# Performance work log

Measured on AMD Instinct MI355X. Metric: run time of the kernel, lower is better.

The kernel has to match this reference:

```python
import jax, jax.numpy as jnp
import numpy as np

B, T, DIM = 2, 2048, 1024
H, HKV, D = 16, 4, 64
ROPE_DIMS = 32
ROPE_BASE = 10000.0


def fake_quant(w, n_bits):
    # per-output-row absmax symmetric fake quantization with STE
    half = 2 ** (n_bits - 1)
    w_max = jnp.maximum(jnp.max(jnp.abs(w), axis=1, keepdims=True), 1e-5)
    w_int = jnp.clip(jnp.round(w / w_max * half), -half, half - 1)
    w_q = w_int / half * w_max
    return w + jax.lax.stop_gradient(w_q - w)


def rms_norm(x):
    eps = jnp.finfo(x.dtype).eps
    return x * jax.lax.rsqrt(jnp.mean(x * x, axis=-1, keepdims=True) + eps)


def rope_tables(seq_len, dtype):
    inv_freq = 1.0 / (ROPE_BASE ** (jnp.arange(0, ROPE_DIMS, 2, dtype=jnp.float32) / ROPE_DIMS))
    t = jnp.arange(seq_len, dtype=jnp.float32)
    freqs = t[:, None] * inv_freq[None, :]  # [T, rope_dims/2]
    return jnp.cos(freqs).astype(dtype)[None, None], jnp.sin(freqs).astype(dtype)[None, None]


def apply_rotary(x, cos, sin):
    # partial rotary: rotate first ROPE_DIMS dims, pass the rest through
    x_rope, x_pass = x[..., :ROPE_DIMS], x[..., ROPE_DIMS:]
    half = ROPE_DIMS // 2
    x1, x2 = x_rope[..., :half], x_rope[..., half:]
    rot = jnp.concatenate([x1 * cos + x2 * sin, -x1 * sin + x2 * cos], axis=-1)
    return jnp.concatenate([rot, x_pass], axis=-1)


def setup_inputs() -> dict:
    key = jax.random.key(0)
    ks = jax.random.split(key, 5)
    kv_dim = HKV * D
    return {
        "x": jax.random.normal(ks[0], (B, T, DIM), dtype=jnp.float32),
        "w_q": jax.random.normal(ks[1], (DIM, DIM), dtype=jnp.float32) * 0.02,
        "w_k": jax.random.normal(ks[2], (kv_dim, DIM), dtype=jnp.float32) * 0.02,
        "w_v": jax.random.normal(ks[3], (kv_dim, DIM), dtype=jnp.float32) * 0.02,
        "w_proj": jax.random.normal(ks[4], (DIM, DIM), dtype=jnp.float32) * 0.02,
        "q_gain": jnp.full((H,), 1.5, dtype=jnp.float32),
    }


def reference(x, w_q, w_k, w_v, w_proj, q_gain):
    bsz, seqlen, dim = x.shape
    group = H // HKV

    # quantized (STE) projections
    q = x @ fake_quant(w_q, 6).T        # [B, T, DIM]
    k = x @ fake_quant(w_k, 6).T        # [B, T, HKV*D]
    v = x @ fake_quant(w_v, 5).T        # [B, T, HKV*D]

    q = q.reshape(bsz, seqlen, H, D).transpose(0, 2, 1, 3)    # [B, H, T, D]
    k = k.reshape(bsz, seqlen, HKV, D).transpose(0, 2, 1, 3)  # [B, HKV, T, D]
    v = v.reshape(bsz, seqlen, HKV, D).transpose(0, 2, 1, 3)  # [B, HKV, T, D]

    q = rms_norm(q)
    k = rms_norm(k)

    cos, sin = rope_tables(seqlen, q.dtype)
    q = apply_rotary(q, cos, sin)
    k = apply_rotary(k, cos, sin)

    q = q * q_gain.astype(q.dtype)[None, :, None, None]

    # grouped-query causal attention; scores kept in grouped [B,HKV,g,T,T] layout
    qg = q.reshape(bsz, HKV, group, seqlen, D)
    scores = jnp.einsum('bhgqd,bhkd->bhgqk', qg, k) / jnp.sqrt(jnp.asarray(D, q.dtype))
    causal = jnp.tril(jnp.ones((seqlen, seqlen), dtype=bool))
    scores = jnp.where(causal[None, None, None], scores, jnp.asarray(-jnp.inf, scores.dtype))
    att = jax.nn.softmax(scores, axis=-1)
    y = jnp.einsum('bhgqk,bhkd->bhgqd', att, v)               # [B, HKV, g, T, D]

    # xsa: orthogonalize y against normalized v (per kv head group)
    y_g = y.transpose(0, 3, 1, 2, 4)                           # [B, T, HKV, g, D]
    v_t = v.transpose(0, 2, 1, 3)                              # [B, T, HKV, D]
    vn = v_t / jnp.maximum(jnp.linalg.norm(v_t, axis=-1, keepdims=True), 1e-12)
    vn = vn[..., None, :]                                      # [B, T, HKV, 1, D]
    proj = jnp.sum(y_g * vn, axis=-1, keepdims=True) * vn
    y_out = (y_g - proj).reshape(bsz, seqlen, dim)

    return y_out @ fake_quant(w_proj, 5).T
```

## Files before the change

kernel.cpp:

```cpp
#include <hip/hip_runtime.h>
#include <math.h>

typedef unsigned short u16;
typedef __attribute__((ext_vector_type(8))) short short8;
typedef __attribute__((ext_vector_type(4))) float float4v;
typedef __attribute__((ext_vector_type(4))) u16 ushort4v;

namespace {
constexpr int kT    = 2048;
constexpr int kDim  = 1024;
constexpr int kH    = 16;
constexpr int kHKV  = 4;
constexpr int kD    = 64;
constexpr int kTok  = 4096;
constexpr int kQKVN = 1536;
}

__device__ __forceinline__ u16 f2bf(float f) {
  unsigned int u = __builtin_bit_cast(unsigned int, f);
  u = (u + 0x7FFFu + ((u >> 16) & 1u)) >> 16;
  return (u16)u;
}

__global__ __launch_bounds__(256) void prep_kernel(
    const float* __restrict__ x,
    const float* __restrict__ w_q, const float* __restrict__ w_k,
    const float* __restrict__ w_v, const float* __restrict__ w_proj,
    u16* __restrict__ xb, u16* __restrict__ wqkv, u16* __restrict__ wpq,
    float2* __restrict__ ropetab)
{
  __shared__ float red[4];
  const int bid = blockIdx.x, tid = threadIdx.x;

  if (bid < 128) {
    const int idx = bid * 256 + tid;
    const int t = idx >> 4, i = idx & 15;
    const float fr = (float)t * powf(10000.0f, -(float)i * (1.0f / 16.0f));
    ropetab[idx] = make_float2(cosf(fr), sinf(fr));
    return;
  }
  if (bid < 2176) {
    const size_t i = ((size_t)(bid - 128) * 256 + tid) * 8;
    const float4 a = *(const float4*)(x + i);
    const float4 b = *(const float4*)(x + i + 4);
    short8 r;
    r[0] = (short)f2bf(a.x); r[1] = (short)f2bf(a.y);
    r[2] = (short)f2bf(a.z); r[3] = (short)f2bf(a.w);
    r[4] = (short)f2bf(b.x); r[5] = (short)f2bf(b.y);
    r[6] = (short)f2bf(b.z); r[7] = (short)f2bf(b.w);
    *(short8*)(xb + i) = r;
    return;
  }
  const int rid = bid - 2176;
  const float* src; u16* dst; float halfv;
  if (rid < 1024)      { src = w_q    + (size_t)rid * 1024;          dst = wqkv + (size_t)rid * 1024;          halfv = 32.0f; }
  else if (rid < 1280) { src = w_k    + (size_t)(rid - 1024) * 1024; dst = wqkv + (size_t)rid * 1024;          halfv = 32.0f; }
  else if (rid < 1536) { src = w_v    + (size_t)(rid - 1280) * 1024; dst = wqkv + (size_t)rid * 1024;          halfv = 16.0f; }
  else                 { src = w_proj + (size_t)(rid - 1536) * 1024; dst = wpq  + (size_t)(rid - 1536) * 1024; halfv = 16.0f; }

  const float4 v4 = *(const float4*)(src + tid * 4);
  float mx = fmaxf(fmaxf(fabsf(v4.x), fabsf(v4.y)), fmaxf(fabsf(v4.z), fabsf(v4.w)));
  #pragma unroll
  for (int m = 1; m < 64; m <<= 1) mx = fmaxf(mx, __shfl_xor(mx, m));
  if ((tid & 63) == 0) red[tid >> 6] = mx;
  __syncthreads();
  mx = fmaxf(fmaxf(red[0], red[1]), fmaxf(red[2], red[3]));
  const float wmax = fmaxf(mx, 1e-5f);
  const float inv_half = 1.0f / halfv;
  const float vals[4] = {v4.x, v4.y, v4.z, v4.w};
  ushort4v o;
  #pragma unroll
  for (int j = 0; j < 4; ++j) {
    float r = rintf(vals[j] / wmax * halfv);
    r = fminf(fmaxf(r, -halfv), halfv - 1.0f);
    o[j] = f2bf(r * inv_half * wmax);
  }
  *(ushort4v*)(dst + tid * 4) = o;
}

#define GEMM_CORE(A_, W_, K_, NCOL0_)                                          \
  __shared__ u16 As[128][32];                                                  \
  __shared__ u16 Bs[64][32];                                                   \
  const int tid = threadIdx.x;                                                 \
  const int lane = tid & 63, wv = tid >> 6;                                    \
  const int n = lane & 15, quad = lane >> 4;                                   \
  const int wm = wv * 32;                                                      \
  const int m0 = blockIdx.y * 128;                                             \
  const int sr = tid >> 2, sc = (tid & 3) * 8;                                 \
  const int scs = sc ^ ((sr & 3) * 8);                                         \
  float4v acc[2][4];                                                           \
  _Pragma("unroll")                                                            \
  for (int mi = 0; mi < 2; ++mi)                                               \
    _Pragma("unroll")                                                          \
    for (int ni = 0; ni < 4; ++ni) {                                           \
      acc[mi][ni][0]=0.f; acc[mi][ni][1]=0.f;                                  \
      acc[mi][ni][2]=0.f; acc[mi][ni][3]=0.f; }                                \
  short8 a0r, a1r, b0r;                                                        \
  a0r = *(const short8*)(A_ + (size_t)(m0 + sr) * K_ + sc);                    \
  a1r = *(const short8*)(A_ + (size_t)(m0 + sr + 64) * K_ + sc);               \
  b0r = *(const short8*)(W_ + (size_t)(NCOL0_ + sr) * K_ + sc);                \
  for (int k0 = 0; k0 < K_; k0 += 32) {                                        \
    __syncthreads();                                                           \
    *(short8*)&As[sr][scs] = a0r;  *(short8*)&As[sr + 64][scs] = a1r;          \
    *(short8*)&Bs[sr][scs] = b0r;                                              \
    __syncthreads();                                                           \
    if (k0 + 32 < K_) {                                                        \
      a0r = *(const short8*)(A_ + (size_t)(m0 + sr) * K_ + k0 + 32 + sc);      \
      a1r = *(const short8*)(A_ + (size_t)(m0 + sr + 64) * K_ + k0 + 32 + sc); \
      b0r = *(const short8*)(W_ + (size_t)(NCOL0_ + sr) * K_ + k0 + 32 + sc);  \
    }                                                                          \
    short8 af[2], bf[4];                                                       \
    _Pragma("unroll")                                                          \
    for (int mi = 0; mi < 2; ++mi)                                             \
      af[mi] = *(const short8*)&As[wm + mi * 16 + n][(quad * 8) ^ ((n & 3) * 8)]; \
    _Pragma("unroll")                                                          \
    for (int ni = 0; ni < 4; ++ni)                                             \
      bf[ni] = *(const short8*)&Bs[ni * 16 + n][(quad * 8) ^ ((n & 3) * 8)];   \
    _Pragma("unroll")                                                          \
    for (int mi = 0; mi < 2; ++mi)                                             \
      _Pragma("unroll")                                                        \
      for (int ni = 0; ni < 4; ++ni)                                           \
        acc[mi][ni] = __builtin_amdgcn_mfma_f32_16x16x32_bf16(af[mi], bf[ni], acc[mi][ni], 0, 0, 0); \
  }

__global__ __launch_bounds__(256) void gemm_qkv(
    const u16* __restrict__ A, const u16* __restrict__ W,
    const float2* __restrict__ ropetab, const float* __restrict__ q_gain,
    u16* __restrict__ qh, u16* __restrict__ kh,
    u16* __restrict__ vT, float* __restrict__ vcmp)
{
  GEMM_CORE(A, W, kDim, (int)(blockIdx.x * 64))

  const int p = blockIdx.x;
  const int rbase = m0 + wm;
  const int bI = rbase >> 11;

  if (p < 20) {
    const float gain = (p < 16) ? q_gain[p] * 0.125f : 1.0f;
    u16* dst = (p < 16) ? qh + ((size_t)(bI * kH + p) * kT) * kD
                        : kh + ((size_t)(bI * kHKV + (p - 16)) * kT) * kD;
    #pragma unroll
    for (int mi = 0; mi < 2; ++mi)
      #pragma unroll
      for (int i = 0; i < 4; ++i) {
        const int row = rbase + mi * 16 + quad * 4 + i;
        const int t = row & (kT - 1);
        float v[4];
        #pragma unroll
        for (int ni = 0; ni < 4; ++ni) v[ni] = acc[mi][ni][i];
        float ss = v[0]*v[0] + v[1]*v[1] + v[2]*v[2] + v[3]*v[3];
        #pragma unroll
        for (int m = 1; m < 16; m <<= 1) ss += __shfl_xor(ss, m);
        const float rr = 1.0f / sqrtf(ss * (1.0f / 64.0f) + 1.1920929e-7f);
        #pragma unroll
        for (int ni = 0; ni < 4; ++ni) v[ni] *= rr;
        const float2 cs = ropetab[t * 16 + n];
        const float r0 =  v[0] * cs.x + v[1] * cs.y;
        const float r1 = -v[0] * cs.y + v[1] * cs.x;
        v[0] = r0; v[1] = r1;
        #pragma unroll
        for (int ni = 0; ni < 4; ++ni)
          dst[(size_t)t * kD + ni * 16 + n] = f2bf(v[ni] * gain);
      }
  } else {
    const int kvh = p - 20;
    u16* vTb = vT + ((size_t)(bI * kHKV + kvh) * kD) * kT;
    #pragma unroll
    for (int mi = 0; mi < 2; ++mi) {
      const int t0 = (rbase + mi * 16 + quad * 4) & (kT - 1);
      #pragma unroll
      for (int ni = 0; ni < 4; ++ni) {
        const int d = ni * 16 + n;
        ushort4v pk;
        pk[0] = f2bf(acc[mi][ni][0]); pk[1] = f2bf(acc[mi][ni][1]);
        pk[2] = f2bf(acc[mi][ni][2]); pk[3] = f2bf(acc[mi][ni][3]);
        *(ushort4v*)(vTb + (size_t)d * kT + t0) = pk;
        #pragma unroll
        for (int i = 0; i < 4; ++i)
          vcmp[(size_t)(rbase + mi * 16 + quad * 4 + i) * (kHKV * kD) + kvh * kD + d] = acc[mi][ni][i];
      }
    }
  }
}

__global__ __launch_bounds__(256) void gemm_out(
    const u16* __restrict__ A, const u16* __restrict__ W,
    float* __restrict__ C)
{
  GEMM_CORE(A, W, kDim, (int)(blockIdx.x * 64))
  const int n0 = blockIdx.x * 64;
  #pragma unroll
  for (int mi = 0; mi < 2; ++mi)
    #pragma unroll
    for (int ni = 0; ni < 4; ++ni)
      #pragma unroll
      for (int i = 0; i < 4; ++i)
        C[(size_t)(m0 + wm + mi * 16 + quad * 4 + i) * kDim + n0 + ni * 16 + n] = acc[mi][ni][i];
}

__global__ __launch_bounds__(256) void attn_mfma(
    const u16* __restrict__ qh, const u16* __restrict__ kh,
    const u16* __restrict__ vT, const float* __restrict__ vcmp,
    u16* __restrict__ yo)
{
  __shared__ u16 ks[64][64];
  __shared__ u16 vs[64][64];
  __shared__ u16 ps[4][16][64];

  const int tid = threadIdx.x;
  const int lane = tid & 63, wq = tid >> 6;
  const int n = lane & 15, quad = lane >> 4;
  const int p = blockIdx.x;
  const int h = blockIdx.y, b = blockIdx.z;
  const int kv = h >> 2;
  const int tiles[2] = {p, 31 - p};
  const u16* kbase = kh + ((size_t)(b * kHKV + kv) * kT) * kD;
  const u16* vbase = vT + ((size_t)(b * kHKV + kv) * kD) * kT;

  short8 qa[2][2];
  {
    const u16* qb = qh + ((size_t)(b * kH + h) * kT) * kD;
    #pragma unroll
    for (int u = 0; u < 2; ++u) {
      const size_t row = (size_t)(tiles[u] * 64 + wq * 16 + n) * kD;
      qa[u][0] = *(const short8*)(qb + row + quad * 8);
      qa[u][1] = *(const short8*)(qb + row + 32 + quad * 8);
    }
  }

  const int sr = tid >> 3;
  const int sc = (tid & 7) * 8;
  const int scs = sc ^ ((sr & 7) * 8);

  float l_r[2] = {0.0f, 0.0f};
  float4v acc[2][4];
  #pragma unroll
  for (int u = 0; u < 2; ++u)
    #pragma unroll
    for (int g = 0; g < 4; ++g) { acc[u][g][0]=0.f; acc[u][g][1]=0.f; acc[u][g][2]=0.f; acc[u][g][3]=0.f; }

  short8 kr0, kr1, vr0, vr1;
  auto loadKV = [&](int kt) {
    kr0 = *(const short8*)(kbase + (size_t)(kt * 64 + sr) * kD + sc);
    kr1 = *(const short8*)(kbase + (size_t)(kt * 64 + sr + 32) * kD + sc);
    vr0 = *(const short8*)(vbase + (size_t)sr * kT + kt * 64 + sc);
    vr1 = *(const short8*)(vbase + (size_t)(sr + 32) * kT + kt * 64 + sc);
  };

  auto process = [&](int u, int kt) {
    float4v s[4];
    #pragma unroll
    for (int g = 0; g < 4; ++g) { s[g][0]=0.f; s[g][1]=0.f; s[g][2]=0.f; s[g][3]=0.f; }
    #pragma unroll
    for (int g = 0; g < 4; ++g) {
      const short8 kb0 = *(const short8*)&ks[g * 16 + n][(quad * 8) ^ ((n & 7) * 8)];
      s[g] = __builtin_amdgcn_mfma_f32_16x16x32_bf16(kb0, qa[u][0], s[g], 0, 0, 0);
      const short8 kb1 = *(const short8*)&ks[g * 16 + n][(32 + quad * 8) ^ ((n & 7) * 8)];
      s[g] = __builtin_amdgcn_mfma_f32_16x16x32_bf16(kb1, qa[u][1], s[g], 0, 0, 0);
    }
    if (kt == tiles[u]) {
      const int mloc = wq * 16 + n;
      #pragma unroll
      for (int g = 0; g < 4; ++g)
        #pragma unroll
        for (int i = 0; i < 4; ++i)
          if (g * 16 + quad * 4 + i > mloc) s[g][i] = -__builtin_inff();
    }
    float pf[4][4]; float rs = 0.0f;
    #pragma unroll
    for (int g = 0; g < 4; ++g)
      #pragma unroll
      for (int i = 0; i < 4; ++i) { pf[g][i] = __expf(s[g][i] - 12.0f); rs += pf[g][i]; }
    rs += __shfl_xor(rs, 16);
    rs += __shfl_xor(rs, 32);
    l_r[u] += rs;
    #pragma unroll
    for (int g = 0; g < 4; ++g) {
      ushort4v pk;
      pk[0] = f2bf(pf[g][0]); pk[1] = f2bf(pf[g][1]);
      pk[2] = f2bf(pf[g][2]); pk[3] = f2bf(pf[g][3]);
      *(ushort4v*)&ps[wq][n][(g * 16 + quad * 4) ^ ((n & 7) * 8)] = pk;
    }
    const short8 pb0 = *(const short8*)&ps[wq][n][(quad * 8) ^ ((n & 7) * 8)];
    const short8 pb1 = *(const short8*)&ps[wq][n][(32 + quad * 8) ^ ((n & 7) * 8)];
    #pragma unroll
    for (int g = 0; g < 4; ++g) {
      const short8 vb0 = *(const short8*)&vs[g * 16 + n][(quad * 8) ^ ((n & 7) * 8)];
      acc[u][g] = __builtin_amdgcn_mfma_f32_16x16x32_bf16(vb0, pb0, acc[u][g], 0, 0, 0);
      const short8 vb1 = *(const short8*)&vs[g * 16 + n][(32 + quad * 8) ^ ((n & 7) * 8)];
      acc[u][g] = __builtin_amdgcn_mfma_f32_16x16x32_bf16(vb1, pb1, acc[u][g], 0, 0, 0);
    }
  };

  const int kmax = tiles[1];
  loadKV(0);
  for (int kt = 0; kt <= kmax; ++kt) {
    __syncthreads();
    *(short8*)&ks[sr][scs]      = kr0;
    *(short8*)&ks[sr + 32][scs] = kr1;
    *(short8*)&vs[sr][scs]      = vr0;
    *(short8*)&vs[sr + 32][scs] = vr1;
    __syncthreads();
    if (kt < kmax) loadKV(kt + 1);
    process(1, kt);
    if (kt <= tiles[0]) process(0, kt);
  }

  #pragma unroll
  for (int u = 0; u < 2; ++u) {
    const int tok = b * kT + tiles[u] * 64 + wq * 16 + n;
    const float invl = 1.0f / l_r[u];
    float4 vv[4]; float nn = 0.0f, syr = 0.0f;
    #pragma unroll
    for (int g = 0; g < 4; ++g) {
      vv[g] = *(const float4*)(vcmp + (size_t)tok * (kHKV * kD) + kv * kD + g * 16 + quad * 4);
      nn  += vv[g].x * vv[g].x + vv[g].y * vv[g].y + vv[g].z * vv[g].z + vv[g].w * vv[g].w;
      syr += acc[u][g][0] * vv[g].x + acc[u][g][1] * vv[g].y + acc[u][g][2] * vv[g].z + acc[u][g][3] * vv[g].w;
    }
    nn  += __shfl_xor(nn, 16);  nn  += __shfl_xor(nn, 32);
    syr += __shfl_xor(syr, 16); syr += __shfl_xor(syr, 32);
    const float inv = 1.0f / fmaxf(sqrtf(nn), 1e-12f);
    const float coef = syr * invl * inv * inv;
    #pragma unroll
    for (int g = 0; g < 4; ++g) {
      const float vf[4] = {vv[g].x, vv[g].y, vv[g].z, vv[g].w};
      ushort4v ow;
      #pragma unroll
      for (int i = 0; i < 4; ++i)
        ow[i] = f2bf(acc[u][g][i] * invl - coef * vf[i]);
      *(ushort4v*)(yo + (size_t)tok * kDim + h * kD + g * 16 + quad * 4) = ow;
    }
  }
}

extern "C" void kernel_launch(void* const* d_in, const int* in_sizes, int n_in,
                              void* d_out, int out_size, void* d_ws, size_t ws_size,
                              hipStream_t stream) {
  (void)in_sizes; (void)n_in; (void)out_size; (void)ws_size;
  const float* x      = (const float*)d_in[0];
  const float* w_q    = (const float*)d_in[1];
  const float* w_k    = (const float*)d_in[2];
  const float* w_v    = (const float*)d_in[3];
  const float* w_proj = (const float*)d_in[4];
  const float* q_gain = (const float*)d_in[5];

  char* wsb = (char*)d_ws;
  u16* wqkv = (u16*)wsb;  wsb += (size_t)1536 * 1024 * 2;
  u16* wpq  = (u16*)wsb;  wsb += (size_t)1024 * 1024 * 2;
  u16* xb   = (u16*)wsb;  wsb += (size_t)kTok * kDim * 2;
  u16* qh   = (u16*)wsb;  wsb += (size_t)kTok * kDim * 2;
  u16* khb  = (u16*)wsb;  wsb += (size_t)kTok * kHKV * kD * 2;
  u16* vTb  = (u16*)wsb;  wsb += (size_t)kTok * kHKV * kD * 2;
  u16* yo   = (u16*)wsb;  wsb += (size_t)kTok * kDim * 2;
  float* vcmp = (float*)wsb; wsb += (size_t)kTok * kHKV * kD * 4;
  float2* ropetab = (float2*)wsb; wsb += (size_t)kT * 16 * sizeof(float2);

  prep_kernel<<<4736, 256, 0, stream>>>(x, w_q, w_k, w_v, w_proj,
                                        xb, wqkv, wpq, ropetab);

  gemm_qkv<<<dim3(24, 32), 256, 0, stream>>>(xb, wqkv, ropetab, q_gain,
                                             qh, khb, vTb, vcmp);

  attn_mfma<<<dim3(16, kH, 2), 256, 0, stream>>>(qh, khb, vTb, vcmp, yo);

  gemm_out<<<dim3(16, 32), 256, 0, stream>>>(yo, wpq, (float*)d_out);
}
```

Baseline: 167.4 us.

## Enlarge GEMM tiles to 128x128 with 2x2 wave layout and packed bf16 conversion

Both projection GEMMs move from a 128x64 block tile to a 128x128 tile, with the four waves arranged 2x2 so each computes a 64x64 subtile. This raises reuse per LDS load and halves the number of blocks. Epilogue index math is adjusted so each wave derives its head column. Separately, the bf16 conversions now use the packed two-float hardware conversion helper instead of the manual rounding per element. In exchange there are more accumulator registers per thread and fewer blocks (384 and 256) on a large-CU GPU, which could hurt occupancy and load balance.

```diff
diff --git a/kernel.cpp b/kernel.cpp
--- a/kernel.cpp
+++ b/kernel.cpp
@@ -1,4 +1,5 @@
 #include <hip/hip_runtime.h>
+#include <hip/hip_bf16.h>
 #include <math.h>
 
 typedef unsigned short u16;
@@ -13,13 +14,20 @@
 constexpr int kHKV  = 4;
 constexpr int kD    = 64;
 constexpr int kTok  = 4096;
-constexpr int kQKVN = 1536;
 }
 
 __device__ __forceinline__ u16 f2bf(float f) {
   unsigned int u = __builtin_bit_cast(unsigned int, f);
   u = (u + 0x7FFFu + ((u >> 16) & 1u)) >> 16;
   return (u16)u;
+}
+__device__ __forceinline__ unsigned pk2(float a, float b) {
+  __hip_bfloat162 h = __float22bfloat162_rn(make_float2(a, b));
+  unsigned u; __builtin_memcpy(&u, &h, 4);
+  return u;
+}
+__device__ __forceinline__ uint2 pack4(float a, float b, float c, float d) {
+  return make_uint2(pk2(a, b), pk2(c, d));
 }
 
 __global__ __launch_bounds__(256) void prep_kernel(
@@ -78,49 +86,51 @@
   *(ushort4v*)(dst + tid * 4) = o;
 }
 
-#define GEMM_CORE(A_, W_, K_, NCOL0_)                                          \
+#define GEMM128_CORE(A_, W_, K_)                                               \
   __shared__ u16 As[128][32];                                                  \
-  __shared__ u16 Bs[64][32];                                                   \
+  __shared__ u16 Bs[128][32];                                                  \
   const int tid = threadIdx.x;                                                 \
   const int lane = tid & 63, wv = tid >> 6;                                    \
   const int n = lane & 15, quad = lane >> 4;                                   \
-  const int wm = wv * 32;                                                      \
-  const int m0 = blockIdx.y * 128;                                             \
+  const int wm = (wv & 1) * 64, wn = (wv >> 1) * 64;                           \
+  const int m0 = blockIdx.y * 128, n0 = blockIdx.x * 128;                      \
   const int sr = tid >> 2, sc = (tid & 3) * 8;                                 \
   const int scs = sc ^ ((sr & 3) * 8);                                         \
-  float4v acc[2][4];                                                           \
+  float4v acc[4][4];                                                           \
   _Pragma("unroll")                                                            \
-  for (int mi = 0; mi < 2; ++mi)                                               \
+  for (int mi = 0; mi < 4; ++mi)                                               \
     _Pragma("unroll")                                                          \
     for (int ni = 0; ni < 4; ++ni) {                                           \
       acc[mi][ni][0]=0.f; acc[mi][ni][1]=0.f;                                  \
       acc[mi][ni][2]=0.f; acc[mi][ni][3]=0.f; }                                \
-  short8 a0r, a1r, b0r;                                                        \
+  short8 a0r, a1r, b0r, b1r;                                                   \
   a0r = *(const short8*)(A_ + (size_t)(m0 + sr) * K_ + sc);                    \
   a1r = *(const short8*)(A_ + (size_t)(m0 + sr + 64) * K_ + sc);               \
-  b0r = *(const short8*)(W_ + (size_t)(NCOL0_ + sr) * K_ + sc);                \
+  b0r = *(const short8*)(W_ + (size_t)(n0 + sr) * K_ + sc);                    \
+  b1r = *(const short8*)(W_ + (size_t)(n0 + sr + 64) * K_ + sc);               \
   for (int k0 = 0; k0 < K_; k0 += 32) {                                        \
     __syncthreads();                                                           \
     *(short8*)&As[sr][scs] = a0r;  *(short8*)&As[sr + 64][scs] = a1r;          \
-    *(short8*)&Bs[sr][scs] = b0r;                                              \
+    *(short8*)&Bs[sr][scs] = b0r;  *(short8*)&Bs[sr + 64][scs] = b1r;          \
     __syncthreads();                                                           \
     if (k0 + 32 < K_) {                                                        \
       a0r = *(const short8*)(A_ + (size_t)(m0 + sr) * K_ + k0 + 32 + sc);      \
       a1r = *(const short8*)(A_ + (size_t)(m0 + sr + 64) * K_ + k0 + 32 + sc); \
-      b0r = *(const short8*)(W_ + (size_t)(NCOL0_ + sr) * K_ + k0 + 32 + sc);  \
+      b0r = *(const short8*)(W_ + (size_t)(n0 + sr) * K_ + k0 + 32 + sc);      \
+      b1r = *(const short8*)(W_ + (size_t)(n0 + sr + 64) * K_ + k0 + 32 + sc); \
     }                                                                          \
-    short8 af[2], bf[4];                                                       \
+    short8 af[4], bfr[4];                                                      \
     _Pragma("unroll")                                                          \
-    for (int mi = 0; mi < 2; ++mi)                                             \
+    for (int mi = 0; mi < 4; ++mi)                                             \
       af[mi] = *(const short8*)&As[wm + mi * 16 + n][(quad * 8) ^ ((n & 3) * 8)]; \
     _Pragma("unroll")                                                          \
     for (int ni = 0; ni < 4; ++ni)                                             \
-      bf[ni] = *(const short8*)&Bs[ni * 16 + n][(quad * 8) ^ ((n & 3) * 8)];   \
+      bfr[ni] = *(const short8*)&Bs[wn + ni * 16 + n][(quad * 8) ^ ((n & 3) * 8)]; \
     _Pragma("unroll")                                                          \
-    for (int mi = 0; mi < 2; ++mi)                                             \
+    for (int mi = 0; mi < 4; ++mi)                                             \
       _Pragma("unroll")                                                        \
       for (int ni = 0; ni < 4; ++ni)                                           \
-        acc[mi][ni] = __builtin_amdgcn_mfma_f32_16x16x32_bf16(af[mi], bf[ni], acc[mi][ni], 0, 0, 0); \
+        acc[mi][ni] = __builtin_amdgcn_mfma_f32_16x16x32_bf16(af[mi], bfr[ni], acc[mi][ni], 0, 0, 0); \
   }
 
 __global__ __launch_bounds__(256) void gemm_qkv(
@@ -129,18 +139,18 @@
     u16* __restrict__ qh, u16* __restrict__ kh,
     u16* __restrict__ vT, float* __restrict__ vcmp)
 {
-  GEMM_CORE(A, W, kDim, (int)(blockIdx.x * 64))
-
-  const int p = blockIdx.x;
+  GEMM128_CORE(A, W, kDim)
+
+  const int hcol = (n0 + wn) >> 6;
   const int rbase = m0 + wm;
   const int bI = rbase >> 11;
 
-  if (p < 20) {
-    const float gain = (p < 16) ? q_gain[p] * 0.125f : 1.0f;
-    u16* dst = (p < 16) ? qh + ((size_t)(bI * kH + p) * kT) * kD
-                        : kh + ((size_t)(bI * kHKV + (p - 16)) * kT) * kD;
-    #pragma unroll
-    for (int mi = 0; mi < 2; ++mi)
+  if (hcol < 20) {
+    const float gain = (hcol < 16) ? q_gain[hcol] * 0.125f : 1.0f;
+    u16* dst = (hcol < 16) ? qh + ((size_t)(bI * kH + hcol) * kT) * kD
+                           : kh + ((size_t)(bI * kHKV + (hcol - 16)) * kT) * kD;
+    #pragma unroll
+    for (int mi = 0; mi < 4; ++mi)
       #pragma unroll
       for (int i = 0; i < 4; ++i) {
         const int row = rbase + mi * 16 + quad * 4 + i;
@@ -163,18 +173,16 @@
           dst[(size_t)t * kD + ni * 16 + n] = f2bf(v[ni] * gain);
       }
   } else {
-    const int kvh = p - 20;
+    const int kvh = hcol - 20;
     u16* vTb = vT + ((size_t)(bI * kHKV + kvh) * kD) * kT;
     #pragma unroll
-    for (int mi = 0; mi < 2; ++mi) {
+    for (int mi = 0; mi < 4; ++mi) {
       const int t0 = (rbase + mi * 16 + quad * 4) & (kT - 1);
       #pragma unroll
       for (int ni = 0; ni < 4; ++ni) {
         const int d = ni * 16 + n;
-        ushort4v pk;
-        pk[0] = f2bf(acc[mi][ni][0]); pk[1] = f2bf(acc[mi][ni][1]);
-        pk[2] = f2bf(acc[mi][ni][2]); pk[3] = f2bf(acc[mi][ni][3]);
-        *(ushort4v*)(vTb + (size_t)d * kT + t0) = pk;
+        *(uint2*)(vTb + (size_t)d * kT + t0) =
+            pack4(acc[mi][ni][0], acc[mi][ni][1], acc[mi][ni][2], acc[mi][ni][3]);
         #pragma unroll
         for (int i = 0; i < 4; ++i)
           vcmp[(size_t)(rbase + mi * 16 + quad * 4 + i) * (kHKV * kD) + kvh * kD + d] = acc[mi][ni][i];
@@ -187,15 +195,14 @@
     const u16* __restrict__ A, const u16* __restrict__ W,
     float* __restrict__ C)
 {
-  GEMM_CORE(A, W, kDim, (int)(blockIdx.x * 64))
-  const int n0 = blockIdx.x * 64;
-  #pragma unroll
-  for (int mi = 0; mi < 2; ++mi)
+  GEMM128_CORE(A, W, kDim)
+  #pragma unroll
+  for (int mi = 0; mi < 4; ++mi)
     #pragma unroll
     for (int ni = 0; ni < 4; ++ni)
       #pragma unroll
       for (int i = 0; i < 4; ++i)
-        C[(size_t)(m0 + wm + mi * 16 + quad * 4 + i) * kDim + n0 + ni * 16 + n] = acc[mi][ni][i];
+        C[(size_t)(m0 + wm + mi * 16 + quad * 4 + i) * kDim + n0 + wn + ni * 16 + n] = acc[mi][ni][i];
 }
 
 __global__ __launch_bounds__(256) void attn_mfma(
@@ -275,12 +282,9 @@
     rs += __shfl_xor(rs, 32);
     l_r[u] += rs;
     #pragma unroll
-    for (int g = 0; g < 4; ++g) {
-      ushort4v pk;
-      pk[0] = f2bf(pf[g][0]); pk[1] = f2bf(pf[g][1]);
-      pk[2] = f2bf(pf[g][2]); pk[3] = f2bf(pf[g][3]);
-      *(ushort4v*)&ps[wq][n][(g * 16 + quad * 4) ^ ((n & 7) * 8)] = pk;
-    }
+    for (int g = 0; g < 4; ++g)
+      *(uint2*)&ps[wq][n][(g * 16 + quad * 4) ^ ((n & 7) * 8)] =
+          pack4(pf[g][0], pf[g][1], pf[g][2], pf[g][3]);
     const short8 pb0 = *(const short8*)&ps[wq][n][(quad * 8) ^ ((n & 7) * 8)];
     const short8 pb1 = *(const short8*)&ps[wq][n][(32 + quad * 8) ^ ((n & 7) * 8)];
     #pragma unroll
@@ -322,14 +326,12 @@
     const float inv = 1.0f / fmaxf(sqrtf(nn), 1e-12f);
     const float coef = syr * invl * inv * inv;
     #pragma unroll
-    for (int g = 0; g < 4; ++g) {
-      const float vf[4] = {vv[g].x, vv[g].y, vv[g].z, vv[g].w};
-      ushort4v ow;
-      #pragma unroll
-      for (int i = 0; i < 4; ++i)
-        ow[i] = f2bf(acc[u][g][i] * invl - coef * vf[i]);
-      *(ushort4v*)(yo + (size_t)tok * kDim + h * kD + g * 16 + quad * 4) = ow;
-    }
+    for (int g = 0; g < 4; ++g)
+      *(uint2*)(yo + (size_t)tok * kDim + h * kD + g * 16 + quad * 4) =
+          pack4(acc[u][g][0] * invl - coef * vv[g].x,
+                acc[u][g][1] * invl - coef * vv[g].y,
+                acc[u][g][2] * invl - coef * vv[g].z,
+                acc[u][g][3] * invl - coef * vv[g].w);
   }
 }
 
@@ -358,10 +360,10 @@
   prep_kernel<<<4736, 256, 0, stream>>>(x, w_q, w_k, w_v, w_proj,
                                         xb, wqkv, wpq, ropetab);
 
-  gemm_qkv<<<dim3(24, 32), 256, 0, stream>>>(xb, wqkv, ropetab, q_gain,
+  gemm_qkv<<<dim3(12, 32), 256, 0, stream>>>(xb, wqkv, ropetab, q_gain,
                                              qh, khb, vTb, vcmp);
 
   attn_mfma<<<dim3(16, kH, 2), 256, 0, stream>>>(qh, khb, vTb, vcmp, yo);
 
-  gemm_out<<<dim3(16, 32), 256, 0, stream>>>(yo, wpq, (float*)d_out);
-}
+  gemm_out<<<dim3(8, 32), 256, 0, stream>>>(yo, wpq, (float*)d_out);
+}
```

New measurement: 170.5 us. No clear change (+1.8%).

## Load GEMM tiles directly into LDS and use packed bf16 conversions

Applied to the files above, without the earlier changes.

The shared GEMM core now uses global_load_lds to copy A and W tiles from global memory straight into LDS. This replaces the register-staged prefetch, which needed an extra barrier and a swizzled store, and it drops the XOR swizzle on the LDS reads. Float-to-bf16 conversions in the epilogues and attention kernel now use the packed two-wide hardware conversion. The trade-off is that the register double-buffering that overlapped global loads with MFMA is gone, and the unswizzled LDS reads may cause bank conflicts.

```diff
diff --git a/kernel.cpp b/kernel.cpp
--- a/kernel.cpp
+++ b/kernel.cpp
@@ -1,4 +1,5 @@
 #include <hip/hip_runtime.h>
+#include <hip/hip_bf16.h>
 #include <math.h>
 
 typedef unsigned short u16;
@@ -13,13 +14,26 @@
 constexpr int kHKV  = 4;
 constexpr int kD    = 64;
 constexpr int kTok  = 4096;
-constexpr int kQKVN = 1536;
 }
 
 __device__ __forceinline__ u16 f2bf(float f) {
   unsigned int u = __builtin_bit_cast(unsigned int, f);
   u = (u + 0x7FFFu + ((u >> 16) & 1u)) >> 16;
   return (u16)u;
+}
+__device__ __forceinline__ unsigned pk2(float a, float b) {
+  __hip_bfloat162 h = __float22bfloat162_rn(make_float2(a, b));
+  unsigned u; __builtin_memcpy(&u, &h, 4);
+  return u;
+}
+__device__ __forceinline__ uint2 pack4(float a, float b, float c, float d) {
+  return make_uint2(pk2(a, b), pk2(c, d));
+}
+
+__device__ __forceinline__ void gl_lds16(const u16* g, u16* l) {
+  __builtin_amdgcn_global_load_lds(
+      (const __attribute__((address_space(1))) void*)g,
+      (__attribute__((address_space(3))) void*)l, 16, 0, 0);
 }
 
 __global__ __launch_bounds__(256) void prep_kernel(
@@ -78,7 +92,7 @@
   *(ushort4v*)(dst + tid * 4) = o;
 }
 
-#define GEMM_CORE(A_, W_, K_, NCOL0_)                                          \
+#define GEMM_GL_CORE(A_, W_, K_, NROW0_)                                       \
   __shared__ u16 As[128][32];                                                  \
   __shared__ u16 Bs[64][32];                                                   \
   const int tid = threadIdx.x;                                                 \
@@ -86,8 +100,13 @@
   const int n = lane & 15, quad = lane >> 4;                                   \
   const int wm = wv * 32;                                                      \
   const int m0 = blockIdx.y * 128;                                             \
-  const int sr = tid >> 2, sc = (tid & 3) * 8;                                 \
-  const int scs = sc ^ ((sr & 3) * 8);                                         \
+  const int lr = lane >> 2, lc = (lane & 3) * 8;                               \
+  const u16* gA0 = A_ + (size_t)(m0 + wv * 16 + lr) * K_ + lc;                 \
+  const u16* gA1 = gA0 + (size_t)64 * K_;                                      \
+  const u16* gB  = W_ + (size_t)(NROW0_ + wv * 16 + lr) * K_ + lc;             \
+  u16* lA0 = &As[wv * 16][0];                                                  \
+  u16* lA1 = &As[64 + wv * 16][0];                                             \
+  u16* lB  = &Bs[wv * 16][0];                                                  \
   float4v acc[2][4];                                                           \
   _Pragma("unroll")                                                            \
   for (int mi = 0; mi < 2; ++mi)                                               \
@@ -95,32 +114,24 @@
     for (int ni = 0; ni < 4; ++ni) {                                           \
       acc[mi][ni][0]=0.f; acc[mi][ni][1]=0.f;                                  \
       acc[mi][ni][2]=0.f; acc[mi][ni][3]=0.f; }                                \
-  short8 a0r, a1r, b0r;                                                        \
-  a0r = *(const short8*)(A_ + (size_t)(m0 + sr) * K_ + sc);                    \
-  a1r = *(const short8*)(A_ + (size_t)(m0 + sr + 64) * K_ + sc);               \
-  b0r = *(const short8*)(W_ + (size_t)(NCOL0_ + sr) * K_ + sc);                \
   for (int k0 = 0; k0 < K_; k0 += 32) {                                        \
     __syncthreads();                                                           \
-    *(short8*)&As[sr][scs] = a0r;  *(short8*)&As[sr + 64][scs] = a1r;          \
-    *(short8*)&Bs[sr][scs] = b0r;                                              \
-    __syncthreads();                                                           \
-    if (k0 + 32 < K_) {                                                        \
-      a0r = *(const short8*)(A_ + (size_t)(m0 + sr) * K_ + k0 + 32 + sc);      \
-      a1r = *(const short8*)(A_ + (size_t)(m0 + sr + 64) * K_ + k0 + 32 + sc); \
-      b0r = *(const short8*)(W_ + (size_t)(NCOL0_ + sr) * K_ + k0 + 32 + sc);  \
-    }                                                                          \
-    short8 af[2], bf[4];                                                       \
+    gl_lds16(gA0 + k0, lA0);                                                   \
+    gl_lds16(gA1 + k0, lA1);                                                   \
+    gl_lds16(gB  + k0, lB);                                                    \
+    __syncthreads();                 \
+    short8 af[2], bfr[4];                                                      \
     _Pragma("unroll")                                                          \
     for (int mi = 0; mi < 2; ++mi)                                             \
-      af[mi] = *(const short8*)&As[wm + mi * 16 + n][(quad * 8) ^ ((n & 3) * 8)]; \
+      af[mi] = *(const short8*)&As[wm + mi * 16 + n][quad * 8];                \
     _Pragma("unroll")                                                          \
     for (int ni = 0; ni < 4; ++ni)                                             \
-      bf[ni] = *(const short8*)&Bs[ni * 16 + n][(quad * 8) ^ ((n & 3) * 8)];   \
+      bfr[ni] = *(const short8*)&Bs[ni * 16 + n][quad * 8];                    \
     _Pragma("unroll")                                                          \
     for (int mi = 0; mi < 2; ++mi)                                             \
       _Pragma("unroll")                                                        \
       for (int ni = 0; ni < 4; ++ni)                                           \
-        acc[mi][ni] = __builtin_amdgcn_mfma_f32_16x16x32_bf16(af[mi], bf[ni], acc[mi][ni], 0, 0, 0); \
+        acc[mi][ni] = __builtin_amdgcn_mfma_f32_16x16x32_bf16(af[mi], bfr[ni], acc[mi][ni], 0, 0, 0); \
   }
 
 __global__ __launch_bounds__(256) void gemm_qkv(
@@ -129,7 +140,7 @@
     u16* __restrict__ qh, u16* __restrict__ kh,
     u16* __restrict__ vT, float* __restrict__ vcmp)
 {
-  GEMM_CORE(A, W, kDim, (int)(blockIdx.x * 64))
+  GEMM_GL_CORE(A, W, kDim, (int)(blockIdx.x * 64))
 
   const int p = blockIdx.x;
   const int rbase = m0 + wm;
@@ -171,10 +182,8 @@
       #pragma unroll
       for (int ni = 0; ni < 4; ++ni) {
         const int d = ni * 16 + n;
-        ushort4v pk;
-        pk[0] = f2bf(acc[mi][ni][0]); pk[1] = f2bf(acc[mi][ni][1]);
-        pk[2] = f2bf(acc[mi][ni][2]); pk[3] = f2bf(acc[mi][ni][3]);
-        *(ushort4v*)(vTb + (size_t)d * kT + t0) = pk;
+        *(uint2*)(vTb + (size_t)d * kT + t0) =
+            pack4(acc[mi][ni][0], acc[mi][ni][1], acc[mi][ni][2], acc[mi][ni][3]);
         #pragma unroll
         for (int i = 0; i < 4; ++i)
           vcmp[(size_t)(rbase + mi * 16 + quad * 4 + i) * (kHKV * kD) + kvh * kD + d] = acc[mi][ni][i];
@@ -187,7 +196,7 @@
     const u16* __restrict__ A, const u16* __restrict__ W,
     float* __restrict__ C)
 {
-  GEMM_CORE(A, W, kDim, (int)(blockIdx.x * 64))
+  GEMM_GL_CORE(A, W, kDim, (int)(blockIdx.x * 64))
   const int n0 = blockIdx.x * 64;
   #pragma unroll
   for (int mi = 0; mi < 2; ++mi)
@@ -275,12 +284,9 @@
     rs += __shfl_xor(rs, 32);
     l_r[u] += rs;
     #pragma unroll
-    for (int g = 0; g < 4; ++g) {
-      ushort4v pk;
-      pk[0] = f2bf(pf[g][0]); pk[1] = f2bf(pf[g][1]);
-      pk[2] = f2bf(pf[g][2]); pk[3] = f2bf(pf[g][3]);
-      *(ushort4v*)&ps[wq][n][(g * 16 + quad * 4) ^ ((n & 7) * 8)] = pk;
-    }
+    for (int g = 0; g < 4; ++g)
+      *(uint2*)&ps[wq][n][(g * 16 + quad * 4) ^ ((n & 7) * 8)] =
+          pack4(pf[g][0], pf[g][1], pf[g][2], pf[g][3]);
     const short8 pb0 = *(const short8*)&ps[wq][n][(quad * 8) ^ ((n & 7) * 8)];
     const short8 pb1 = *(const short8*)&ps[wq][n][(32 + quad * 8) ^ ((n & 7) * 8)];
     #pragma unroll
@@ -322,14 +328,12 @@
     const float inv = 1.0f / fmaxf(sqrtf(nn), 1e-12f);
     const float coef = syr * invl * inv * inv;
     #pragma unroll
-    for (int g = 0; g < 4; ++g) {
-      const float vf[4] = {vv[g].x, vv[g].y, vv[g].z, vv[g].w};
-      ushort4v ow;
-      #pragma unroll
-      for (int i = 0; i < 4; ++i)
-        ow[i] = f2bf(acc[u][g][i] * invl - coef * vf[i]);
-      *(ushort4v*)(yo + (size_t)tok * kDim + h * kD + g * 16 + quad * 4) = ow;
-    }
+    for (int g = 0; g < 4; ++g)
+      *(uint2*)(yo + (size_t)tok * kDim + h * kD + g * 16 + quad * 4) =
+          pack4(acc[u][g][0] * invl - coef * vv[g].x,
+                acc[u][g][1] * invl - coef * vv[g].y,
+                acc[u][g][2] * invl - coef * vv[g].z,
+                acc[u][g][3] * invl - coef * vv[g].w);
   }
 }
 
```

Result: no change. 167.8 us (+0.2%).
